# Performance work log

Measured on AMD Instinct MI355X. Metric: run time of the kernel, lower is better.

Reference implementation:

```python
import jax, jax.numpy as jnp
import numpy as np

H = 4  # num_heads in all three MultiheadAttention layers


def _mha(x, valid, Wq, Wk, Wv, Wo, bq, bk, bv, bo):
    """Batched self-attention with key_padding_mask, matching torch MHA math.
    x: [..., L, D]; valid: [..., L] float (1=real token, 0=pad)."""
    lead = x.shape[:-2]
    L, D = x.shape[-2], x.shape[-1]
    dh = D // H
    q = (x @ Wq + bq).reshape(*lead, L, H, dh)
    k = (x @ Wk + bk).reshape(*lead, L, H, dh)
    v = (x @ Wv + bv).reshape(*lead, L, H, dh)
    scores = jnp.einsum('...qhd,...khd->...hqk', q, k) / jnp.sqrt(jnp.asarray(dh, x.dtype))
    neg = jnp.asarray(-1e9, x.dtype)  # finite so fully-masked rows stay NaN-free
    scores = jnp.where(valid[..., None, None, :] > 0, scores, neg)
    a = jax.nn.softmax(scores, axis=-1)
    o = jnp.einsum('...hqk,...khd->...qhd', a, v).reshape(*lead, L, D)
    return o @ Wo + bo


def _masked_mean(x, m):
    # (x * m).sum over sequence / (m.sum + 1e-10); fully-masked -> exact zeros,
    # matching the torch zeros() fallback branch.
    mm = m[..., None]
    return (x * mm).sum(-2) / (mm.sum(-2) + 1e-10)


def setup_inputs() -> dict:
    key = jax.random.key(0)
    B, S, N, W, D = 16, 8, 16, 64, 256
    ks = jax.random.split(key, 16)
    inp = {
        'word_embeddings': jax.random.normal(ks[0], (B, S, N, W, D), dtype=jnp.float32),
        'attention_mask': jax.random.randint(ks[1], (B, S, N, W), 0, 2).astype(jnp.int32),
    }
    i = 2
    for lvl in 'wsc':  # word / sentence / section attention params
        for p in ('Wq', 'Wk', 'Wv', 'Wo'):
            inp[lvl + p] = 0.02 * jax.random.normal(ks[i], (D, D), dtype=jnp.float32)
            i += 1
        for p in ('bq', 'bk', 'bv', 'bo'):
            inp[lvl + p] = jnp.zeros((D,), jnp.float32)
    return inp


def reference(word_embeddings, attention_mask,
              wWq, wWk, wWv, wWo, wbq, wbk, wbv, wbo,
              sWq, sWk, sWv, sWo, sbq, sbk, sbv, sbo,
              cWq, cWk, cWv, cWo, cbq, cbk, cbv, cbo):
    dt = word_embeddings.dtype
    mask = attention_mask.astype(dt)                       # [B,S,N,W]
    # word level: attention within each sentence, then masked mean pooling
    wo = _mha(word_embeddings, mask, wWq, wWk, wWv, wWo, wbq, wbk, wbv, wbo)
    sent = _masked_mean(wo, mask)                          # [B,S,N,D]
    # sentence level
    sent_mask = (mask.sum(-1) > 0).astype(dt)              # [B,S,N]
    so = _mha(sent, sent_mask, sWq, sWk, sWv, sWo, sbq, sbk, sbv, sbo)
    sec = _masked_mean(so, sent_mask)                      # [B,S,D]
    # section level
    sec_mask = (mask.sum((-1, -2)) > 0).astype(dt)         # [B,S]
    co = _mha(sec, sec_mask, cWq, cWk, cWv, cWo, cbq, cbk, cbv, cbo)
    doc = _masked_mean(co, sec_mask)                       # [B,D]
    return doc
```

## Files before the change

kernel.cpp:

```cpp
#include <hip/hip_runtime.h>

constexpr int D = 256;

typedef __attribute__((ext_vector_type(8))) __bf16 bf16x8;
typedef __attribute__((ext_vector_type(4))) float f32x4;

__device__ inline unsigned short f2b(float f) {
    unsigned u = __builtin_bit_cast(unsigned, f);
    u = (u + 0x7fffu + ((u >> 16) & 1u)) >> 16;
    return (unsigned short)u;
}
__device__ inline unsigned cvt_pk_bf16(float lo, float hi) {
    unsigned r;
    asm volatile("v_cvt_pk_bf16_f32 %0, %1, %2" : "=v"(r) : "v"(lo), "v"(hi));
    return r;
}
__device__ inline bf16x8 ld_frag(const void* p) {
    uint4 r = *(const uint4*)p;
    return __builtin_bit_cast(bf16x8, r);
}
template<int CTRL>
__device__ inline float dpp_f(float v) {
    return __builtin_bit_cast(float,
        __builtin_amdgcn_update_dpp(0, __builtin_bit_cast(int, v), CTRL, 0xf, 0xf, true));
}
__device__ inline float rsum16(float v) {
    v += dpp_f<0x121>(v);
    v += dpp_f<0x122>(v);
    v += dpp_f<0x124>(v);
    v += dpp_f<0x128>(v);
    return v;
}
__device__ inline float rmax16(float v) {
    v = fmaxf(v, dpp_f<0x121>(v));
    v = fmaxf(v, dpp_f<0x122>(v));
    v = fmaxf(v, dpp_f<0x124>(v));
    v = fmaxf(v, dpp_f<0x128>(v));
    return v;
}

__global__ void prep_wt3(const float* __restrict__ q0, const float* __restrict__ k0,
                         const float* __restrict__ q1, const float* __restrict__ k1,
                         const float* __restrict__ q2, const float* __restrict__ k2,
                         unsigned short* __restrict__ WT) {
    const int b = blockIdx.x, k = threadIdx.x;
    const int lvl = b >> 9, c = b & 511;
    const float* Wq = (lvl == 0) ? q0 : (lvl == 1) ? q1 : q2;
    const float* Wk = (lvl == 0) ? k0 : (lvl == 1) ? k1 : k2;
    const float* W = (c < 256) ? Wq : Wk;
    WT[(size_t)b * 256 + k] = f2b(W[k * 256 + (c & 255)]);
}

template<int NSUB, typename MT>
__global__ __launch_bounds__(512, 4)
void attn_kernel(const float* __restrict__ X, const MT* __restrict__ Mask,
                 const unsigned short* __restrict__ WT,
                 const float* __restrict__ bq, const float* __restrict__ bk,
                 const float* __restrict__ Wv, const float* __restrict__ Wo,
                 const float* __restrict__ bv, const float* __restrict__ bo,
                 float* __restrict__ Out0, float* __restrict__ Out1)
{
    constexpr int LSUB = 64 / NSUB;
    constexpr int L2S  = (LSUB == 64) ? 6 : (LSUB == 16) ? 4 : 3;
    constexpr int NS   = (NSUB > 1) ? NSUB : 1;

    __shared__ unsigned short sQK[64 * 512];
    __shared__ float sM[64];
    __shared__ float sPart[8][64];
    __shared__ float sCt[NS];
    __shared__ float sAbar[4][64];
    __shared__ float sPP[NS][256];
    __shared__ float sH[2][NS][256];

    const int tid = threadIdx.x;
    const int blk = blockIdx.x;
    const float* Xs = X + (size_t)blk * 64 * D;
    char* sB = (char*)sQK;
    const int lane = tid & 63, w = tid >> 6;
    const int lr = lane & 15, lg = lane >> 4;

    uint2 pk[8];
    {
        const float4* X4 = (const float4*)Xs;
        float4 xv[8];
        #pragma unroll
        for (int j = 0; j < 8; ++j) xv[j] = X4[tid + j * 512];
        if (tid < 64) sM[tid] = (float)Mask[(size_t)blk * 64 + tid];
        #pragma unroll
        for (int j = 0; j < 8; ++j) {
            pk[j].x = cvt_pk_bf16(xv[j].x, xv[j].y);
            pk[j].y = cvt_pk_bf16(xv[j].z, xv[j].w);
            const int row = w + 8 * j;
            *(uint2*)(sB + row * 512 + ((lane * 8) ^ ((row & 7) << 4))) = pk[j];
        }
    }
    __syncthreads();
    if (tid < 64) {
        float v = sM[tid];
        #pragma unroll
        for (int o = 1; o < LSUB; o <<= 1) v += __shfl_xor(v, o);
        if ((tid & (LSUB - 1)) == 0) sCt[tid >> L2S] = v;
    }

    f32x4 acc[4][4];
    {
        const float* bias = (w < 4) ? bq : bk;
        const int fb = (w & 3) * 64;
        #pragma unroll
        for (int m = 0; m < 4; ++m) {
            float4 b4 = *(const float4*)(bias + fb + m * 16 + lg * 4);
            f32x4 bi = {b4.x, b4.y, b4.z, b4.w};
            #pragma unroll
            for (int n = 0; n < 4; ++n) acc[m][n] = bi;
        }
        const unsigned short* wtp = WT + (size_t)(w * 64 + lr) * 256 + lg * 8;
        bf16x8 afn[4];
        #pragma unroll
        for (int m = 0; m < 4; ++m) afn[m] = ld_frag(wtp + m * 16 * 256);
        #pragma unroll 1
        for (int kk = 0; kk < 8; ++kk) {
            bf16x8 af[4];
            #pragma unroll
            for (int m = 0; m < 4; ++m) af[m] = afn[m];
            if (kk < 7) {
                #pragma unroll
                for (int m = 0; m < 4; ++m) afn[m] = ld_frag(wtp + m * 16 * 256 + (kk + 1) * 32);
            }
            bf16x8 bx[4];
            #pragma unroll
            for (int n = 0; n < 4; ++n) {
                int t = n * 16 + lr;
                bx[n] = ld_frag(sB + t * 512 + ((kk * 64 + lg * 16) ^ ((t & 7) << 4)));
            }
            __builtin_amdgcn_s_setprio(1);
            #pragma unroll
            for (int m = 0; m < 4; ++m)
                #pragma unroll
                for (int n = 0; n < 4; ++n)
                    acc[m][n] = __builtin_amdgcn_mfma_f32_16x16x32_bf16(af[m], bx[n], acc[m][n], 0, 0, 0);
            __builtin_amdgcn_s_setprio(0);
        }
    }
    __syncthreads();
    #pragma unroll
    for (int n = 0; n < 4; ++n) {
        int t = n * 16 + lr;
        char* rowp = sB + t * 1024;
        int sw = (t & 7) << 4;
        #pragma unroll
        for (int m = 0; m < 4; ++m) {
            uint2 qk;
            qk.x = cvt_pk_bf16(acc[m][n][0], acc[m][n][1]);
            qk.y = cvt_pk_bf16(acc[m][n][2], acc[m][n][3]);
            *(uint2*)(rowp + ((w * 128 + m * 32 + lg * 8) ^ sw)) = qk;
        }
    }
    __syncthreads();

    {
        const int h = w >> 1, msel = w & 1;
        f32x4 sacc[2][4];
        #pragma unroll
        for (int m = 0; m < 2; ++m)
            #pragma unroll
            for (int n = 0; n < 4; ++n) sacc[m][n] = (f32x4){0.f, 0.f, 0.f, 0.f};
        #pragma unroll
        for (int kk = 0; kk < 2; ++kk) {
            bf16x8 qf[2];
            #pragma unroll
            for (int m = 0; m < 2; ++m) {
                int t = msel * 32 + m * 16 + lr;
                qf[m] = ld_frag(sB + t * 1024 + ((h * 128 + kk * 64 + lg * 16) ^ ((t & 7) << 4)));
            }
            __builtin_amdgcn_s_setprio(1);
            #pragma unroll
            for (int n = 0; n < 4; ++n) {
                int t = n * 16 + lr;
                bf16x8 kf = ld_frag(sB + t * 1024 + ((512 + h * 128 + kk * 64 + lg * 16) ^ ((t & 7) << 4)));
                #pragma unroll
                for (int m = 0; m < 2; ++m)
                    sacc[m][n] = __builtin_amdgcn_mfma_f32_16x16x32_bf16(qf[m], kf, sacc[m][n], 0, 0, 0);
            }
            __builtin_amdgcn_s_setprio(0);
        }
        float mcol[4];
        int csub[4];
        #pragma unroll
        for (int n = 0; n < 4; ++n) {
            mcol[n] = sM[n * 16 + lr];
            csub[n] = (n * 16 + lr) >> L2S;
        }
        constexpr float CE = 0.125f * 1.44269504f;
        float pm[4] = {0.f, 0.f, 0.f, 0.f};
        #pragma unroll
        for (int m = 0; m < 2; ++m)
            #pragma unroll
            for (int r = 0; r < 4; ++r) {
                const int rowtok = msel * 32 + m * 16 + lg * 4 + r;
                const int rsub = rowtok >> L2S;
                float s[4], mx = -3.4e38f;
                #pragma unroll
                for (int n = 0; n < 4; ++n) {
                    float v = sacc[m][n][r];
                    bool ok = (mcol[n] > 0.f);
                    if constexpr (NSUB > 1) ok = ok && (csub[n] == rsub);
                    v = ok ? v : -1e9f;
                    s[n] = v; mx = fmaxf(mx, v);
                }
                mx = rmax16(mx);
                float e[4], se;
                #pragma unroll
                for (int n = 0; n < 4; ++n) e[n] = __builtin_amdgcn_exp2f((s[n] - mx) * CE);
                se = rsum16(((e[0] + e[1]) + (e[2] + e[3])));
                const float wr = sM[rowtok] * __builtin_amdgcn_rcpf(se);
                #pragma unroll
                for (int n = 0; n < 4; ++n) pm[n] += e[n] * wr;
            }
        #pragma unroll
        for (int o = 16; o < 64; o <<= 1)
            #pragma unroll
            for (int n = 0; n < 4; ++n) pm[n] += __shfl_xor(pm[n], o);
        if (lane < 16)
            #pragma unroll
            for (int n = 0; n < 4; ++n) sPart[w][n * 16 + lane] = pm[n];
    }
    __syncthreads();
    if (tid < 256) {
        int h = tid >> 6, j = tid & 63;
        sAbar[h][j] = sPart[2 * h][j] + sPart[2 * h + 1][j];
    }
    __syncthreads();

    if constexpr (NSUB == 1) {
        float zp[4][4];
        #pragma unroll
        for (int h = 0; h < 4; ++h)
            #pragma unroll
            for (int e = 0; e < 4; ++e) zp[h][e] = 0.f;
        #pragma unroll
        for (int j = 0; j < 8; ++j) {
            const int t = w + 8 * j;
            float ab0 = sAbar[0][t], ab1 = sAbar[1][t];
            float ab2 = sAbar[2][t], ab3 = sAbar[3][t];
            float x0 = __builtin_bit_cast(float, pk[j].x << 16);
            float x1 = __builtin_bit_cast(float, pk[j].x & 0xffff0000u);
            float x2 = __builtin_bit_cast(float, pk[j].y << 16);
            float x3 = __builtin_bit_cast(float, pk[j].y & 0xffff0000u);
            zp[0][0] = fmaf(ab0, x0, zp[0][0]); zp[0][1] = fmaf(ab0, x1, zp[0][1]);
            zp[0][2] = fmaf(ab0, x2, zp[0][2]); zp[0][3] = fmaf(ab0, x3, zp[0][3]);
            zp[1][0] = fmaf(ab1, x0, zp[1][0]); zp[1][1] = fmaf(ab1, x1, zp[1][1]);
            zp[1][2] = fmaf(ab1, x2, zp[1][2]); zp[1][3] = fmaf(ab1, x3, zp[1][3]);
            zp[2][0] = fmaf(ab2, x0, zp[2][0]); zp[2][1] = fmaf(ab2, x1, zp[2][1]);
            zp[2][2] = fmaf(ab2, x2, zp[2][2]); zp[2][3] = fmaf(ab2, x3, zp[2][3]);
            zp[3][0] = fmaf(ab3, x0, zp[3][0]); zp[3][1] = fmaf(ab3, x1, zp[3][1]);
            zp[3][2] = fmaf(ab3, x2, zp[3][2]); zp[3][3] = fmaf(ab3, x3, zp[3][3]);
        }
        float* zr = (float*)sB;
        #pragma unroll
        for (int h = 0; h < 4; ++h)
            *(f32x4*)&zr[(w * 4 + h) * 256 + lane * 4] =
                (f32x4){zp[h][0], zp[h][1], zp[h][2], zp[h][3]};
        __syncthreads();
        {
            const int d = tid & 255, hp = (tid >> 8) * 2;
            float a0 = 0.f, a1 = 0.f;
            #pragma unroll
            for (int ww = 0; ww < 8; ++ww) {
                a0 += zr[(ww * 4 + hp) * 256 + d];
                a1 += zr[(ww * 4 + hp + 1) * 256 + d];
            }
            float* Zo = Out0 + (size_t)blk * 1024;
            Zo[hp * 256 + d] = a0;
            Zo[(hp + 1) * 256 + d] = a1;
        }
        if (tid == 0) Out1[blk] = sCt[0];
    } else {
        float* zpf = (float*)sB;
        const int d = tid & 255, rh = tid >> 8;
        constexpr int HT = LSUB / 2;
        #pragma unroll
        for (int s = 0; s < NSUB; ++s) {
            float zz[4] = {0.f, 0.f, 0.f, 0.f};
            const int t0 = s * LSUB + rh * HT;
            #pragma unroll
            for (int t = 0; t < HT; ++t) {
                float xv = Xs[(size_t)(t0 + t) * 256 + d];
                #pragma unroll
                for (int h = 0; h < 4; ++h) zz[h] = fmaf(sAbar[h][t0 + t], xv, zz[h]);
            }
            #pragma unroll
            for (int h = 0; h < 4; ++h) zpf[((rh * NSUB + s) * 4 + h) * 256 + d] = zz[h];
        }
        __syncthreads();
        {
            const int n = tid & 255, g = tid >> 8, h = n >> 6;
            float pa[NSUB];
            #pragma unroll
            for (int s = 0; s < NSUB; ++s) pa[s] = 0.f;
            for (int dc = 0; dc < 128; dc += 8) {
                float wv[8];
                #pragma unroll
                for (int q = 0; q < 8; ++q) wv[q] = Wv[(size_t)(g * 128 + dc + q) * 256 + n];
                #pragma unroll
                for (int s = 0; s < NSUB; ++s)
                    #pragma unroll
                    for (int q = 0; q < 8; ++q) {
                        int dd = g * 128 + dc + q;
                        float zv = zpf[(s * 4 + h) * 256 + dd] + zpf[((NSUB + s) * 4 + h) * 256 + dd];
                        pa[s] = fmaf(zv, wv[q], pa[s]);
                    }
            }
            #pragma unroll
            for (int s = 0; s < NSUB; ++s) sH[g][s][n] = pa[s];
        }
        __syncthreads();
        for (int i = tid; i < NSUB * 256; i += 512) {
            int s = i >> 8, nn = i & 255;
            sPP[s][nn] = sH[0][s][nn] + sH[1][s][nn] + sCt[s] * bv[nn];
        }
        __syncthreads();
        {
            const int n = tid & 255, g = tid >> 8;
            float pa[NSUB];
            #pragma unroll
            for (int s = 0; s < NSUB; ++s) pa[s] = 0.f;
            for (int dc = 0; dc < 128; dc += 8) {
                float wo[8];
                #pragma unroll
                for (int q = 0; q < 8; ++q) wo[q] = Wo[(size_t)(g * 128 + dc + q) * 256 + n];
                #pragma unroll
                for (int s = 0; s < NSUB; ++s) {
                    const float* pp = &sPP[s][g * 128 + dc];
                    #pragma unroll
                    for (int q = 0; q < 8; ++q) pa[s] = fmaf(pp[q], wo[q], pa[s]);
                }
            }
            #pragma unroll
            for (int s = 0; s < NSUB; ++s) sH[g][s][n] = pa[s];
        }
        __syncthreads();
        for (int i = tid; i < NSUB * 256; i += 512) {
            int s = i >> 8, nn = i & 255;
            float c = sCt[s];
            Out0[(size_t)(blk * NSUB + s) * 256 + nn] =
                (c > 0.f) ? ((sH[0][s][nn] + sH[1][s][nn]) / c + bo[nn]) : 0.f;
        }
        if (tid < NSUB && Out1) Out1[blk * NSUB + tid] = (sCt[tid] > 0.f) ? 1.f : 0.f;
    }
}

__global__ __launch_bounds__(512, 2)
void apply2(const float* __restrict__ Z, const float* __restrict__ Cnt,
            const float* __restrict__ Wv, const float* __restrict__ Wo,
            const float* __restrict__ bv, const float* __restrict__ bo,
            float* __restrict__ Out, float* __restrict__ MaskOut)
{
    constexpr int SPB = 8;
    __shared__ float sZ[SPB][4][256];
    __shared__ float sPP[SPB][256];
    __shared__ float sH[2][SPB][256];
    __shared__ float sCt[SPB];

    const int tid = threadIdx.x;
    const int s0 = blockIdx.x * SPB;
    {
        const float4* Zf = (const float4*)(Z + (size_t)s0 * 1024);
        float4* sZf = (float4*)sZ;
        #pragma unroll
        for (int k = 0; k < 4; ++k) sZf[tid + k * 512] = Zf[tid + k * 512];
        if (tid < SPB) sCt[tid] = Cnt[s0 + tid];
    }
    __syncthreads();

    const int n = tid & 255, g = tid >> 8, h = n >> 6;

    {
        float pa[SPB] = {};
        for (int dc = 0; dc < 128; dc += 16) {
            float wv[16];
            #pragma unroll
            for (int q = 0; q < 16; ++q) wv[q] = Wv[(size_t)(g * 128 + dc + q) * 256 + n];
            #pragma unroll
            for (int s = 0; s < SPB; ++s) {
                const float4* zp4 = (const float4*)&sZ[s][h][g * 128 + dc];
                #pragma unroll
                for (int q4 = 0; q4 < 4; ++q4) {
                    float4 zv = zp4[q4];
                    pa[s] = fmaf(zv.x, wv[q4 * 4 + 0], pa[s]);
                    pa[s] = fmaf(zv.y, wv[q4 * 4 + 1], pa[s]);
                    pa[s] = fmaf(zv.z, wv[q4 * 4 + 2], pa[s]);
                    pa[s] = fmaf(zv.w, wv[q4 * 4 + 3], pa[s]);
                }
            }
        }
        #pragma unroll
        for (int s = 0; s < SPB; ++s) sH[g][s][n] = pa[s];
    }
    __syncthreads();
    for (int i = tid; i < SPB * 256; i += 512) {
        int s = i >> 8, nn = i & 255;
        sPP[s][nn] = sH[0][s][nn] + sH[1][s][nn] + sCt[s] * bv[nn];
    }
    __syncthreads();
    {
        float pa[SPB] = {};
        for (int dc = 0; dc < 128; dc += 16) {
            float wo[16];
            #pragma unroll
            for (int q = 0; q < 16; ++q) wo[q] = Wo[(size_t)(g * 128 + dc + q) * 256 + n];
            #pragma unroll
            for (int s = 0; s < SPB; ++s) {
                const float4* pp = (const float4*)&sPP[s][g * 128 + dc];
                #pragma unroll
                for (int q4 = 0; q4 < 4; ++q4) {
                    float4 pv = pp[q4];
                    pa[s] = fmaf(pv.x, wo[q4 * 4 + 0], pa[s]);
                    pa[s] = fmaf(pv.y, wo[q4 * 4 + 1], pa[s]);
                    pa[s] = fmaf(pv.z, wo[q4 * 4 + 2], pa[s]);
                    pa[s] = fmaf(pv.w, wo[q4 * 4 + 3], pa[s]);
                }
            }
        }
        #pragma unroll
        for (int s = 0; s < SPB; ++s) sH[g][s][n] = pa[s];
    }
    __syncthreads();
    for (int i = tid; i < SPB * 256; i += 512) {
        int s = i >> 8, nn = i & 255;
        float c = sCt[s];
        Out[(size_t)(s0 + s) * 256 + nn] = (c > 0.f) ? ((sH[0][s][nn] + sH[1][s][nn]) / c + bo[nn]) : 0.f;
    }
    if (tid < SPB && MaskOut) MaskOut[s0 + tid] = (sCt[tid] > 0.f) ? 1.f : 0.f;
}

extern "C" void kernel_launch(void* const* d_in, const int* in_sizes, int n_in,
                              void* d_out, int out_size, void* d_ws, size_t ws_size,
                              hipStream_t stream)
{
    const float* emb  = (const float*)d_in[0];
    const int*  amask = (const int*)d_in[1];
    const float* W[24];
    for (int i = 0; i < 24; ++i) W[i] = (const float*)d_in[2 + i];

    char* ws = (char*)d_ws;
    unsigned short* WT = (unsigned short*)ws;
    float* zbuf  = (float*)(ws + 3 * 256 * 1024);
    float* cnt   = zbuf + 2048 * 1024;
    float* sent  = cnt + 2048;
    float* smask = sent + 2048 * 256;
    float* sec   = smask + 2048;
    float* cmask = sec + 128 * 256;
    float* out   = (float*)d_out;

    prep_wt3<<<dim3(1536), dim3(256), 0, stream>>>(W[0], W[1], W[8], W[9], W[16], W[17], WT);

    attn_kernel<1, int><<<dim3(2048), dim3(512), 0, stream>>>(
        emb, amask, WT, W[4], W[5], nullptr, nullptr, nullptr, nullptr, zbuf, cnt);
    apply2<<<dim3(256), dim3(512), 0, stream>>>(
        zbuf, cnt, W[2], W[3], W[6], W[7], sent, smask);

    attn_kernel<4, float><<<dim3(32), dim3(512), 0, stream>>>(
        sent, smask, WT + 512 * 256, W[12], W[13], W[10], W[11], W[14], W[15], sec, cmask);

    attn_kernel<8, float><<<dim3(2), dim3(512), 0, stream>>>(
        sec, cmask, WT + 2 * 512 * 256, W[20], W[21], W[18], W[19], W[22], W[23], out, nullptr);
}
```

Before: 176.5 us.

## Split sentence/section attention into per-sequence tail kernel with more blocks

Replaces the templated multi-sequence attention for the sentence and section levels with a dedicated tail kernel that handles one short sequence (16 or 8 tokens) per block. The grid grows from 32 and 2 blocks to 128 and 16, and the QK projection now covers only 16 rows instead of 64 padded ones. The word-level kernel becomes a non-templated specialization and issues its first weight-fragment loads before the barrier. The intent is to cut the latency of the serial, under-occupied tail stages. In exchange, the Wv and Wo weights are re-read by many more blocks.

```diff
diff --git a/kernel.cpp b/kernel.cpp
--- a/kernel.cpp
+++ b/kernel.cpp
@@ -38,6 +38,7 @@
     v = fmaxf(v, dpp_f<0x128>(v));
     return v;
 }
+constexpr float CE = 0.125f * 1.44269504f;
 
 __global__ void prep_wt3(const float* __restrict__ q0, const float* __restrict__ k0,
                          const float* __restrict__ q1, const float* __restrict__ k1,
@@ -51,26 +52,17 @@
     WT[(size_t)b * 256 + k] = f2b(W[k * 256 + (c & 255)]);
 }
 
-template<int NSUB, typename MT>
 __global__ __launch_bounds__(512, 4)
-void attn_kernel(const float* __restrict__ X, const MT* __restrict__ Mask,
-                 const unsigned short* __restrict__ WT,
-                 const float* __restrict__ bq, const float* __restrict__ bk,
-                 const float* __restrict__ Wv, const float* __restrict__ Wo,
-                 const float* __restrict__ bv, const float* __restrict__ bo,
-                 float* __restrict__ Out0, float* __restrict__ Out1)
+void word_attn(const float* __restrict__ X, const int* __restrict__ Mask,
+               const unsigned short* __restrict__ WT,
+               const float* __restrict__ bq, const float* __restrict__ bk,
+               float* __restrict__ Zout, float* __restrict__ Cnt)
 {
-    constexpr int LSUB = 64 / NSUB;
-    constexpr int L2S  = (LSUB == 64) ? 6 : (LSUB == 16) ? 4 : 3;
-    constexpr int NS   = (NSUB > 1) ? NSUB : 1;
-
     __shared__ unsigned short sQK[64 * 512];
     __shared__ float sM[64];
     __shared__ float sPart[8][64];
-    __shared__ float sCt[NS];
     __shared__ float sAbar[4][64];
-    __shared__ float sPP[NS][256];
-    __shared__ float sH[2][NS][256];
+    __shared__ float sCt;
 
     const int tid = threadIdx.x;
     const int blk = blockIdx.x;
@@ -94,12 +86,16 @@
             *(uint2*)(sB + row * 512 + ((lane * 8) ^ ((row & 7) << 4))) = pk[j];
         }
     }
+    const unsigned short* wtp = WT + (size_t)(w * 64 + lr) * 256 + lg * 8;
+    bf16x8 afn[4];
+    #pragma unroll
+    for (int m = 0; m < 4; ++m) afn[m] = ld_frag(wtp + m * 16 * 256);
     __syncthreads();
     if (tid < 64) {
         float v = sM[tid];
         #pragma unroll
-        for (int o = 1; o < LSUB; o <<= 1) v += __shfl_xor(v, o);
-        if ((tid & (LSUB - 1)) == 0) sCt[tid >> L2S] = v;
+        for (int o = 1; o < 64; o <<= 1) v += __shfl_xor(v, o);
+        if (tid == 0) sCt = v;
     }
 
     f32x4 acc[4][4];
@@ -113,10 +109,6 @@
             #pragma unroll
             for (int n = 0; n < 4; ++n) acc[m][n] = bi;
         }
-        const unsigned short* wtp = WT + (size_t)(w * 64 + lr) * 256 + lg * 8;
-        bf16x8 afn[4];
-        #pragma unroll
-        for (int m = 0; m < 4; ++m) afn[m] = ld_frag(wtp + m * 16 * 256);
         #pragma unroll 1
         for (int kk = 0; kk < 8; ++kk) {
             bf16x8 af[4];
@@ -184,27 +176,19 @@
             __builtin_amdgcn_s_setprio(0);
         }
         float mcol[4];
-        int csub[4];
-        #pragma unroll
-        for (int n = 0; n < 4; ++n) {
-            mcol[n] = sM[n * 16 + lr];
-            csub[n] = (n * 16 + lr) >> L2S;
-        }
-        constexpr float CE = 0.125f * 1.44269504f;
+        #pragma unroll
+        for (int n = 0; n < 4; ++n) mcol[n] = sM[n * 16 + lr];
         float pm[4] = {0.f, 0.f, 0.f, 0.f};
         #pragma unroll
         for (int m = 0; m < 2; ++m)
             #pragma unroll
             for (int r = 0; r < 4; ++r) {
                 const int rowtok = msel * 32 + m * 16 + lg * 4 + r;
-                const int rsub = rowtok >> L2S;
                 float s[4], mx = -3.4e38f;
                 #pragma unroll
                 for (int n = 0; n < 4; ++n) {
                     float v = sacc[m][n][r];
-                    bool ok = (mcol[n] > 0.f);
-                    if constexpr (NSUB > 1) ok = ok && (csub[n] == rsub);
-                    v = ok ? v : -1e9f;
+                    v = (mcol[n] > 0.f) ? v : -1e9f;
                     s[n] = v; mx = fmaxf(mx, v);
                 }
                 mx = rmax16(mx);
@@ -231,122 +215,48 @@
     }
     __syncthreads();
 
-    if constexpr (NSUB == 1) {
-        float zp[4][4];
-        #pragma unroll
-        for (int h = 0; h < 4; ++h)
-            #pragma unroll
-            for (int e = 0; e < 4; ++e) zp[h][e] = 0.f;
-        #pragma unroll
-        for (int j = 0; j < 8; ++j) {
-            const int t = w + 8 * j;
-            float ab0 = sAbar[0][t], ab1 = sAbar[1][t];
-            float ab2 = sAbar[2][t], ab3 = sAbar[3][t];
-            float x0 = __builtin_bit_cast(float, pk[j].x << 16);
-            float x1 = __builtin_bit_cast(float, pk[j].x & 0xffff0000u);
-            float x2 = __builtin_bit_cast(float, pk[j].y << 16);
-            float x3 = __builtin_bit_cast(float, pk[j].y & 0xffff0000u);
-            zp[0][0] = fmaf(ab0, x0, zp[0][0]); zp[0][1] = fmaf(ab0, x1, zp[0][1]);
-            zp[0][2] = fmaf(ab0, x2, zp[0][2]); zp[0][3] = fmaf(ab0, x3, zp[0][3]);
-            zp[1][0] = fmaf(ab1, x0, zp[1][0]); zp[1][1] = fmaf(ab1, x1, zp[1][1]);
-            zp[1][2] = fmaf(ab1, x2, zp[1][2]); zp[1][3] = fmaf(ab1, x3, zp[1][3]);
-            zp[2][0] = fmaf(ab2, x0, zp[2][0]); zp[2][1] = fmaf(ab2, x1, zp[2][1]);
-            zp[2][2] = fmaf(ab2, x2, zp[2][2]); zp[2][3] = fmaf(ab2, x3, zp[2][3]);
-            zp[3][0] = fmaf(ab3, x0, zp[3][0]); zp[3][1] = fmaf(ab3, x1, zp[3][1]);
-            zp[3][2] = fmaf(ab3, x2, zp[3][2]); zp[3][3] = fmaf(ab3, x3, zp[3][3]);
-        }
-        float* zr = (float*)sB;
-        #pragma unroll
-        for (int h = 0; h < 4; ++h)
-            *(f32x4*)&zr[(w * 4 + h) * 256 + lane * 4] =
-                (f32x4){zp[h][0], zp[h][1], zp[h][2], zp[h][3]};
-        __syncthreads();
-        {
-            const int d = tid & 255, hp = (tid >> 8) * 2;
-            float a0 = 0.f, a1 = 0.f;
-            #pragma unroll
-            for (int ww = 0; ww < 8; ++ww) {
-                a0 += zr[(ww * 4 + hp) * 256 + d];
-                a1 += zr[(ww * 4 + hp + 1) * 256 + d];
-            }
-            float* Zo = Out0 + (size_t)blk * 1024;
-            Zo[hp * 256 + d] = a0;
-            Zo[(hp + 1) * 256 + d] = a1;
-        }
-        if (tid == 0) Out1[blk] = sCt[0];
-    } else {
-        float* zpf = (float*)sB;
-        const int d = tid & 255, rh = tid >> 8;
-        constexpr int HT = LSUB / 2;
-        #pragma unroll
-        for (int s = 0; s < NSUB; ++s) {
-            float zz[4] = {0.f, 0.f, 0.f, 0.f};
-            const int t0 = s * LSUB + rh * HT;
-            #pragma unroll
-            for (int t = 0; t < HT; ++t) {
-                float xv = Xs[(size_t)(t0 + t) * 256 + d];
-                #pragma unroll
-                for (int h = 0; h < 4; ++h) zz[h] = fmaf(sAbar[h][t0 + t], xv, zz[h]);
-            }
-            #pragma unroll
-            for (int h = 0; h < 4; ++h) zpf[((rh * NSUB + s) * 4 + h) * 256 + d] = zz[h];
-        }
-        __syncthreads();
-        {
-            const int n = tid & 255, g = tid >> 8, h = n >> 6;
-            float pa[NSUB];
-            #pragma unroll
-            for (int s = 0; s < NSUB; ++s) pa[s] = 0.f;
-            for (int dc = 0; dc < 128; dc += 8) {
-                float wv[8];
-                #pragma unroll
-                for (int q = 0; q < 8; ++q) wv[q] = Wv[(size_t)(g * 128 + dc + q) * 256 + n];
-                #pragma unroll
-                for (int s = 0; s < NSUB; ++s)
-                    #pragma unroll
-                    for (int q = 0; q < 8; ++q) {
-                        int dd = g * 128 + dc + q;
-                        float zv = zpf[(s * 4 + h) * 256 + dd] + zpf[((NSUB + s) * 4 + h) * 256 + dd];
-                        pa[s] = fmaf(zv, wv[q], pa[s]);
-                    }
-            }
-            #pragma unroll
-            for (int s = 0; s < NSUB; ++s) sH[g][s][n] = pa[s];
-        }
-        __syncthreads();
-        for (int i = tid; i < NSUB * 256; i += 512) {
-            int s = i >> 8, nn = i & 255;
-            sPP[s][nn] = sH[0][s][nn] + sH[1][s][nn] + sCt[s] * bv[nn];
-        }
-        __syncthreads();
-        {
-            const int n = tid & 255, g = tid >> 8;
-            float pa[NSUB];
-            #pragma unroll
-            for (int s = 0; s < NSUB; ++s) pa[s] = 0.f;
-            for (int dc = 0; dc < 128; dc += 8) {
-                float wo[8];
-                #pragma unroll
-                for (int q = 0; q < 8; ++q) wo[q] = Wo[(size_t)(g * 128 + dc + q) * 256 + n];
-                #pragma unroll
-                for (int s = 0; s < NSUB; ++s) {
-                    const float* pp = &sPP[s][g * 128 + dc];
-                    #pragma unroll
-                    for (int q = 0; q < 8; ++q) pa[s] = fmaf(pp[q], wo[q], pa[s]);
-                }
-            }
-            #pragma unroll
-            for (int s = 0; s < NSUB; ++s) sH[g][s][n] = pa[s];
-        }
-        __syncthreads();
-        for (int i = tid; i < NSUB * 256; i += 512) {
-            int s = i >> 8, nn = i & 255;
-            float c = sCt[s];
-            Out0[(size_t)(blk * NSUB + s) * 256 + nn] =
-                (c > 0.f) ? ((sH[0][s][nn] + sH[1][s][nn]) / c + bo[nn]) : 0.f;
-        }
-        if (tid < NSUB && Out1) Out1[blk * NSUB + tid] = (sCt[tid] > 0.f) ? 1.f : 0.f;
-    }
+    float zp[4][4];
+    #pragma unroll
+    for (int h = 0; h < 4; ++h)
+        #pragma unroll
+        for (int e = 0; e < 4; ++e) zp[h][e] = 0.f;
+    #pragma unroll
+    for (int j = 0; j < 8; ++j) {
+        const int t = w + 8 * j;
+        float ab0 = sAbar[0][t], ab1 = sAbar[1][t];
+        float ab2 = sAbar[2][t], ab3 = sAbar[3][t];
+        float x0 = __builtin_bit_cast(float, pk[j].x << 16);
+        float x1 = __builtin_bit_cast(float, pk[j].x & 0xffff0000u);
+        float x2 = __builtin_bit_cast(float, pk[j].y << 16);
+        float x3 = __builtin_bit_cast(float, pk[j].y & 0xffff0000u);
+        zp[0][0] = fmaf(ab0, x0, zp[0][0]); zp[0][1] = fmaf(ab0, x1, zp[0][1]);
+        zp[0][2] = fmaf(ab0, x2, zp[0][2]); zp[0][3] = fmaf(ab0, x3, zp[0][3]);
+        zp[1][0] = fmaf(ab1, x0, zp[1][0]); zp[1][1] = fmaf(ab1, x1, zp[1][1]);
+        zp[1][2] = fmaf(ab1, x2, zp[1][2]); zp[1][3] = fmaf(ab1, x3, zp[1][3]);
+        zp[2][0] = fmaf(ab2, x0, zp[2][0]); zp[2][1] = fmaf(ab2, x1, zp[2][1]);
+        zp[2][2] = fmaf(ab2, x2, zp[2][2]); zp[2][3] = fmaf(ab2, x3, zp[2][3]);
+        zp[3][0] = fmaf(ab3, x0, zp[3][0]); zp[3][1] = fmaf(ab3, x1, zp[3][1]);
+        zp[3][2] = fmaf(ab3, x2, zp[3][2]); zp[3][3] = fmaf(ab3, x3, zp[3][3]);
+    }
+    float* zr = (float*)sB;
+    #pragma unroll
+    for (int h = 0; h < 4; ++h)
+        *(f32x4*)&zr[(w * 4 + h) * 256 + lane * 4] =
+            (f32x4){zp[h][0], zp[h][1], zp[h][2], zp[h][3]};
+    __syncthreads();
+    {
+        const int d = tid & 255, hp = (tid >> 8) * 2;
+        float a0 = 0.f, a1 = 0.f;
+        #pragma unroll
+        for (int ww = 0; ww < 8; ++ww) {
+            a0 += zr[(ww * 4 + hp) * 256 + d];
+            a1 += zr[(ww * 4 + hp + 1) * 256 + d];
+        }
+        float* Zo = Zout + (size_t)blk * 1024;
+        Zo[hp * 256 + d] = a0;
+        Zo[(hp + 1) * 256 + d] = a1;
+    }
+    if (tid == 0) Cnt[blk] = sCt;
 }
 
 __global__ __launch_bounds__(512, 2)
@@ -433,6 +343,171 @@
     if (tid < SPB && MaskOut) MaskOut[s0 + tid] = (sCt[tid] > 0.f) ? 1.f : 0.f;
 }
 
+template<int LREAL>
+__global__ __launch_bounds__(512, 2)
+void tail_kernel(const float* __restrict__ X, const float* __restrict__ MaskIn,
+                 const unsigned short* __restrict__ WT,
+                 const float* __restrict__ bq, const float* __restrict__ bk,
+                 const float* __restrict__ Wv, const float* __restrict__ Wo,
+                 const float* __restrict__ bv, const float* __restrict__ bo,
+                 float* __restrict__ Out, float* __restrict__ MaskOut)
+{
+    __shared__ unsigned short sX[16 * 256];
+    __shared__ unsigned short sQK[16 * 512];
+    __shared__ float sXF[16][256];
+    __shared__ float sM[16];
+    __shared__ float sAbar[4][16];
+    __shared__ float sZp[2][4][256];
+    __shared__ float sPP[256];
+    __shared__ float sHH[2][256];
+    __shared__ float sCt;
+
+    const int tid = threadIdx.x;
+    const int seq = blockIdx.x;
+    const float* Xs = X + (size_t)seq * LREAL * 256;
+    char* sBX = (char*)sX;
+    char* sBQ = (char*)sQK;
+    const int lane = tid & 63, w = tid >> 6;
+    const int lr = lane & 15, lg = lane >> 4;
+
+    {
+        const float4* X4 = (const float4*)Xs;
+        #pragma unroll
+        for (int j = 0; j < 2; ++j) {
+            int idx = tid + j * 512;
+            int row = idx >> 6, c4 = idx & 63;
+            float4 v = (row < LREAL) ? X4[row * 64 + c4] : (float4){0.f, 0.f, 0.f, 0.f};
+            uint2 p;
+            p.x = cvt_pk_bf16(v.x, v.y);
+            p.y = cvt_pk_bf16(v.z, v.w);
+            *(uint2*)(sBX + row * 512 + ((c4 * 8) ^ ((row & 7) << 4))) = p;
+            *(float4*)&sXF[row][c4 * 4] = v;
+        }
+        if (tid < 16) sM[tid] = (tid < LREAL) ? MaskIn[seq * LREAL + tid] : 0.f;
+    }
+    const unsigned short* wtp = WT + (size_t)(w * 64 + lr) * 256 + lg * 8;
+    bf16x8 afn[4];
+    #pragma unroll
+    for (int m = 0; m < 4; ++m) afn[m] = ld_frag(wtp + m * 16 * 256);
+    __syncthreads();
+    if (tid < 64) {
+        float v = (lane < LREAL) ? sM[lane] : 0.f;
+        v = rsum16(v);
+        if (lane == 0) sCt = v;
+    }
+
+    f32x4 acc[4];
+    {
+        const float* bias = (w < 4) ? bq : bk;
+        const int fb = (w & 3) * 64;
+        #pragma unroll
+        for (int m = 0; m < 4; ++m) {
+            float4 b4 = *(const float4*)(bias + fb + m * 16 + lg * 4);
+            acc[m] = (f32x4){b4.x, b4.y, b4.z, b4.w};
+        }
+        #pragma unroll 1
+        for (int kk = 0; kk < 8; ++kk) {
+            bf16x8 af[4];
+            #pragma unroll
+            for (int m = 0; m < 4; ++m) af[m] = afn[m];
+            if (kk < 7) {
+                #pragma unroll
+                for (int m = 0; m < 4; ++m) afn[m] = ld_frag(wtp + m * 16 * 256 + (kk + 1) * 32);
+            }
+            bf16x8 bx = ld_frag(sBX + lr * 512 + ((kk * 64 + lg * 16) ^ ((lr & 7) << 4)));
+            #pragma unroll
+            for (int m = 0; m < 4; ++m)
+                acc[m] = __builtin_amdgcn_mfma_f32_16x16x32_bf16(af[m], bx, acc[m], 0, 0, 0);
+        }
+    }
+    #pragma unroll
+    for (int m = 0; m < 4; ++m) {
+        uint2 qk;
+        qk.x = cvt_pk_bf16(acc[m][0], acc[m][1]);
+        qk.y = cvt_pk_bf16(acc[m][2], acc[m][3]);
+        *(uint2*)(sBQ + lr * 1024 + ((w * 128 + m * 32 + lg * 8) ^ ((lr & 7) << 4))) = qk;
+    }
+    __syncthreads();
+
+    if (w < 4) {
+        const int h = w;
+        f32x4 sacc = (f32x4){0.f, 0.f, 0.f, 0.f};
+        #pragma unroll
+        for (int kk = 0; kk < 2; ++kk) {
+            bf16x8 qf = ld_frag(sBQ + lr * 1024 + ((h * 128 + kk * 64 + lg * 16) ^ ((lr & 7) << 4)));
+            bf16x8 kf = ld_frag(sBQ + lr * 1024 + ((512 + h * 128 + kk * 64 + lg * 16) ^ ((lr & 7) << 4)));
+            sacc = __builtin_amdgcn_mfma_f32_16x16x32_bf16(qf, kf, sacc, 0, 0, 0);
+        }
+        const float mkey = sM[lr];
+        float t = 0.f;
+        #pragma unroll
+        for (int r = 0; r < 4; ++r) {
+            const int qi = lg * 4 + r;
+            float s = (mkey > 0.f) ? sacc[r] : -1e9f;
+            float mx = rmax16(s);
+            float e = __builtin_amdgcn_exp2f((s - mx) * CE);
+            float se = rsum16(e);
+            t += e * (sM[qi] * __builtin_amdgcn_rcpf(se));
+        }
+        t += __shfl_xor(t, 16);
+        t += __shfl_xor(t, 32);
+        if (lane < 16) sAbar[h][lane] = t;
+    }
+    __syncthreads();
+
+    {
+        const int d = tid & 255, rh = tid >> 8;
+        float zz[4] = {0.f, 0.f, 0.f, 0.f};
+        #pragma unroll
+        for (int t = 0; t < 8; ++t) {
+            const int tok = rh * 8 + t;
+            float xv = sXF[tok][d];
+            #pragma unroll
+            for (int h = 0; h < 4; ++h) zz[h] = fmaf(sAbar[h][tok], xv, zz[h]);
+        }
+        #pragma unroll
+        for (int h = 0; h < 4; ++h) sZp[rh][h][d] = zz[h];
+    }
+    __syncthreads();
+
+    const int n = tid & 255, g = tid >> 8, h = n >> 6;
+    {
+        float pa = 0.f;
+        for (int dc = 0; dc < 128; dc += 16) {
+            float wv[16];
+            #pragma unroll
+            for (int q = 0; q < 16; ++q) wv[q] = Wv[(size_t)(g * 128 + dc + q) * 256 + n];
+            #pragma unroll
+            for (int q = 0; q < 16; ++q) {
+                int dd = g * 128 + dc + q;
+                pa = fmaf(sZp[0][h][dd] + sZp[1][h][dd], wv[q], pa);
+            }
+        }
+        sHH[g][n] = pa;
+    }
+    __syncthreads();
+    if (tid < 256) sPP[tid] = sHH[0][tid] + sHH[1][tid] + sCt * bv[tid];
+    __syncthreads();
+    {
+        float pa = 0.f;
+        for (int dc = 0; dc < 128; dc += 16) {
+            float wo[16];
+            #pragma unroll
+            for (int q = 0; q < 16; ++q) wo[q] = Wo[(size_t)(g * 128 + dc + q) * 256 + n];
+            const float* pp = &sPP[g * 128 + dc];
+            #pragma unroll
+            for (int q = 0; q < 16; ++q) pa = fmaf(pp[q], wo[q], pa);
+        }
+        sHH[g][n] = pa;
+    }
+    __syncthreads();
+    if (tid < 256) {
+        float c = sCt;
+        Out[(size_t)seq * 256 + tid] = (c > 0.f) ? ((sHH[0][tid] + sHH[1][tid]) / c + bo[tid]) : 0.f;
+        if (MaskOut && tid == 0) MaskOut[seq] = (c > 0.f) ? 1.f : 0.f;
+    }
+}
+
 extern "C" void kernel_launch(void* const* d_in, const int* in_sizes, int n_in,
                               void* d_out, int out_size, void* d_ws, size_t ws_size,
                               hipStream_t stream)
@@ -454,14 +529,12 @@
 
     prep_wt3<<<dim3(1536), dim3(256), 0, stream>>>(W[0], W[1], W[8], W[9], W[16], W[17], WT);
 
-    attn_kernel<1, int><<<dim3(2048), dim3(512), 0, stream>>>(
-        emb, amask, WT, W[4], W[5], nullptr, nullptr, nullptr, nullptr, zbuf, cnt);
-    apply2<<<dim3(256), dim3(512), 0, stream>>>(
-        zbuf, cnt, W[2], W[3], W[6], W[7], sent, smask);
-
-    attn_kernel<4, float><<<dim3(32), dim3(512), 0, stream>>>(
+    word_attn<<<dim3(2048), dim3(512), 0, stream>>>(emb, amask, WT, W[4], W[5], zbuf, cnt);
+    apply2<<<dim3(256), dim3(512), 0, stream>>>(zbuf, cnt, W[2], W[3], W[6], W[7], sent, smask);
+
+    tail_kernel<16><<<dim3(128), dim3(512), 0, stream>>>(
         sent, smask, WT + 512 * 256, W[12], W[13], W[10], W[11], W[14], W[15], sec, cmask);
 
-    attn_kernel<8, float><<<dim3(2), dim3(512), 0, stream>>>(
+    tail_kernel<8><<<dim3(16), dim3(512), 0, stream>>>(
         sec, cmask, WT + 2 * 512 * 256, W[20], W[21], W[18], W[19], W[22], W[23], out, nullptr);
 }
```

After: 151.6 us. 1.16x faster.
